# Kernel optimization log

Measured on AMD Instinct MI355X. Metric: run time of the kernel, lower is better.

## Reference

```python
import jax, jax.numpy as jnp
import numpy as np

N = 50000          # num nodes
E = 800000         # num edges (before self loops)
F = 128            # input feature dim
UNITS = 128        # output units
ATT_UNITS = 128    # attention units (Q/K dim)
HEADS = 8


def setup_inputs() -> dict:
    key = jax.random.key(0)
    ks = jax.random.split(key, 6)
    s = 1.0 / np.sqrt(F).astype(np.float32)  # ~glorot scale
    return {
        "x": jax.random.normal(ks[0], (N, F), dtype=jnp.float32),
        "edge_index": jax.random.randint(ks[1], (2, E), 0, N, dtype=jnp.int32),
        "query_kernel": jax.random.normal(ks[2], (F, ATT_UNITS), dtype=jnp.float32) * s,
        "query_bias": jnp.zeros((ATT_UNITS,), jnp.float32),
        "key_kernel": jax.random.normal(ks[3], (F, ATT_UNITS), dtype=jnp.float32) * s,
        "key_bias": jnp.zeros((ATT_UNITS,), jnp.float32),
        "kernel": jax.random.normal(ks[4], (F, UNITS), dtype=jnp.float32) * s,
        "bias": jnp.zeros((UNITS,), jnp.float32),
    }


def segment_softmax(scores, seg, num_segments):
    # scores: [E', H], seg: [E'] -> softmax over edges sharing the same target node, per head
    smax = jax.ops.segment_max(scores, seg, num_segments=num_segments)
    sexp = jnp.exp(scores - smax[seg])
    ssum = jax.ops.segment_sum(sexp, seg, num_segments=num_segments)
    return sexp / ssum[seg]


def reference(x, edge_index, query_kernel, query_bias, key_kernel, key_bias, kernel, bias):
    num_nodes = x.shape[0]
    # add self-loop edges (as in tf_geometric add_self_loop_edge)
    loop = jnp.arange(num_nodes, dtype=edge_index.dtype)
    row = jnp.concatenate([edge_index[0], loop])  # target nodes, [E']
    col = jnp.concatenate([edge_index[1], loop])  # source nodes, [E']

    Q = jax.nn.relu(x @ query_kernel + query_bias)[row]  # [E', A]
    K = jax.nn.relu(x @ key_kernel + key_bias)[col]      # [E', A]
    V = (x @ kernel)[col]                                 # [E', U]

    # split into attention heads: tf.split(..., num_heads, axis=-1)
    Qh = Q.reshape(-1, HEADS, ATT_UNITS // HEADS)
    Kh = K.reshape(-1, HEADS, ATT_UNITS // HEADS)
    att = jnp.sum(Qh * Kh, axis=-1)                       # [E', H]
    alpha = segment_softmax(att, row, num_nodes)          # [E', H]

    # split_value_heads=True: split V into head slices, weight, scatter-add, concat
    Vh = V.reshape(-1, HEADS, UNITS // HEADS)             # [E', H, U/H]
    msg = Vh * alpha[:, :, None]
    out = jax.ops.segment_sum(msg, row, num_segments=num_nodes)  # [N, H, U/H]
    out = out.reshape(num_nodes, UNITS)
    out = out + bias  # use_bias=True, activation=None
    return out
```

## Files before the change

kernel.cpp:

```cpp
#include <hip/hip_runtime.h>
#include <hip/hip_fp16.h>
#include <cstdint>

#define FDIM 128
#define XSTR 136
#define NROWTILE 128
#define WCHUNKS ((FDIM * XSTR * 2) / 1024)
#define CSRS 128

typedef __attribute__((ext_vector_type(8))) _Float16 half8;
typedef __attribute__((ext_vector_type(2))) _Float16 h2;
typedef __attribute__((ext_vector_type(16))) float float16;

#if defined(__has_builtin)
#if __has_builtin(__builtin_amdgcn_fdot2)
#define HAVE_FDOT2 1
#endif
#endif

__device__ __forceinline__ void gload_lds16(const void* g, void* s) {
    __builtin_amdgcn_global_load_lds(
        (const __attribute__((address_space(1))) void*)g,
        (__attribute__((address_space(3))) void*)s, 16, 0, 0);
}

__device__ __forceinline__ h2 as_h2(unsigned u) {
    union { unsigned u; h2 h; } c; c.u = u; return c.h;
}
__device__ __forceinline__ float2 h2_to_f2(unsigned u) {
    __half2 h = *(__half2*)&u;
    return __half22float2(h);
}

__global__ __launch_bounds__(256) void prep_k(
    const float* __restrict__ Wq, const float* __restrict__ Wk,
    const float* __restrict__ Wv, __half* __restrict__ WTH,
    int* __restrict__ deg, int N)
{
    int idx = blockIdx.x * 256 + threadIdx.x;

    if (idx < N) deg[idx] = 0;

    if (idx < 3 * FDIM * FDIM) {
        int mat = idx >> 14;
        int m = idx & 16383;
        int k = m >> 7;
        int nn = m & 127;
        const float* __restrict__ W = (mat == 0) ? Wq : (mat == 1) ? Wk : Wv;
        WTH[(size_t)mat * FDIM * XSTR + nn * XSTR + k] =
            __float2half_rn(W[k * FDIM + nn]);
    }
}

__global__ __launch_bounds__(256) void gemm_edges_k(
    const float* __restrict__ x, const __half* __restrict__ WTH,
    const float* __restrict__ bq, const float* __restrict__ bk,
    const float* __restrict__ bias,
    __half* __restrict__ Qb, uint2* __restrict__ KV,
    const int* __restrict__ ei, int E,
    int* __restrict__ deg, int* __restrict__ csr, int N)
{
    __shared__ __half xs[NROWTILE * XSTR];
    __shared__ __half ws[FDIM * XSTR];

    const int tid  = threadIdx.x;
    const int wave = tid >> 6;
    const int lane = tid & 63;
    const int r0   = blockIdx.x * NROWTILE;

    for (int c = wave; c < WCHUNKS; c += 4)
        gload_lds16((const char*)WTH + c * 1024 + lane * 16, (char*)ws + c * 1024);

    #pragma unroll
    for (int it = 0; it < 16; ++it) {
        int idx = it * 256 + tid;
        int row = idx >> 5;
        int c = (idx & 31) << 2;
        float4 v = make_float4(0.f, 0.f, 0.f, 0.f);
        if (r0 + row < N) v = *(const float4*)(x + (size_t)(r0 + row) * FDIM + c);
        __half h[4] = {__float2half_rn(v.x), __float2half_rn(v.y),
                       __float2half_rn(v.z), __float2half_rn(v.w)};
        *(ushort4*)(xs + row * XSTR + c) = *(ushort4*)h;
    }

    {
        const int NT = gridDim.x * 256;
        const int gtid = blockIdx.x * 256 + tid;
        for (int e = gtid; e < E; e += NT) {
            int row = ei[e];
            int col = ei[E + e];
            int slot = atomicAdd(&deg[row], 1);
            if (slot < CSRS) csr[(row << 7) + slot] = col;
        }
    }

    const int mrow = lane & 31;
    const int half = lane >> 5;
    const int arow = wave * 32 + mrow;

    for (int mat = 0; mat < 3; ++mat) {
        __syncthreads();

        float16 acc[4];
        #pragma unroll
        for (int nt = 0; nt < 4; ++nt)
            #pragma unroll
            for (int r = 0; r < 16; ++r) acc[nt][r] = 0.f;

        #pragma unroll
        for (int ks = 0; ks < 8; ++ks) {
            const int ko = ks * 16 + half * 8;
            half8 ah = *(const half8*)(xs + arow * XSTR + ko);
            #pragma unroll
            for (int nt = 0; nt < 4; ++nt) {
                half8 bh = *(const half8*)(ws + (nt * 32 + mrow) * XSTR + ko);
                acc[nt] = __builtin_amdgcn_mfma_f32_32x32x16_f16(ah, bh, acc[nt], 0, 0, 0);
            }
        }

        __syncthreads();

        const float* bvec = (mat == 0) ? bq : (mat == 1) ? bk : bias;
        #pragma unroll
        for (int nt = 0; nt < 4; ++nt) {
            const int col = nt * 32 + mrow;
            const float bb = bvec[col];
            #pragma unroll
            for (int reg = 0; reg < 16; ++reg) {
                int rl = wave * 32 + (reg & 3) + 8 * (reg >> 2) + 4 * half;
                float v = acc[nt][reg] + bb;
                if (mat < 2) v = fmaxf(v, 0.f);
                ws[rl * XSTR + col] = __float2half_rn(v);
            }
        }
        __syncthreads();

        if (mat == 0) {
            #pragma unroll
            for (int it = 0; it < 8; ++it) {
                int idx = it * 256 + tid;
                int row = idx >> 4;
                int c = (idx & 15) * 8;
                uint4 v = *(const uint4*)(ws + row * XSTR + c);
                if (r0 + row < N)
                    *(uint4*)(Qb + (size_t)(r0 + row) * FDIM + c) = v;
            }
        } else {
            __half* kvh = (__half*)KV;
            const int sub = (mat == 2) ? 2 : 0;
            #pragma unroll
            for (int it = 0; it < 32; ++it) {
                int idx = it * 256 + tid;
                int row = idx >> 6;
                int p = idx & 63;
                unsigned v = *(const unsigned*)(ws + row * XSTR + 2 * p);
                if (r0 + row < N)
                    *(unsigned*)(kvh + (size_t)(r0 + row) * 256 + p * 4 + sub) = v;
            }
        }
        __syncthreads();

        if (mat < 2) {
            const char* wbase = (const char*)(WTH + (size_t)(mat + 1) * FDIM * XSTR);
            for (int c = wave; c < WCHUNKS; c += 4)
                gload_lds16(wbase + c * 1024 + lane * 16, (char*)ws + c * 1024);
        }
    }
}

__global__ __launch_bounds__(256) void aggregate_k(
    const __half* __restrict__ Qb, const uint2* __restrict__ KV,
    const int* __restrict__ deg, const int* __restrict__ csr,
    float* __restrict__ out, int N)
{
    const int lane = threadIdx.x & 63;
    int n = blockIdx.x * 4 + (threadIdx.x >> 6);
    if (n >= N) return;
    n = __builtin_amdgcn_readfirstlane(n);

    int d = __builtin_amdgcn_readfirstlane(deg[n]);
    if (d > CSRS) d = CSRS;
    const int off   = n << 7;
    const int total = d + 1;

    const unsigned qu = *(const unsigned*)(Qb + (size_t)n * FDIM + 2 * lane);
    const h2 q2 = as_h2(qu);
#ifndef HAVE_FDOT2
    const float2 qf = h2_to_f2(qu);
#endif

    float acc0 = 0.f, acc1 = 0.f, lsum = 0.f;

    int idxbuf[8];
    #pragma unroll
    for (int u = 0; u < 8; ++u)
        idxbuf[u] = (u == 0) ? n : ((u < total) ? csr[off + u - 1] : 0);

    for (int t = 0; t < total; t += 8) {
        uint2 kv[8];
        #pragma unroll
        for (int u = 0; u < 8; ++u)
            kv[u] = KV[(((unsigned)idxbuf[u]) << 6) + lane];
        #pragma unroll
        for (int u = 0; u < 8; ++u) {
            int nx = t + 8 + u;
            idxbuf[u] = (nx < total) ? csr[off + nx - 1] : 0;
        }
        #pragma unroll
        for (int u = 0; u < 8; ++u) {
#ifdef HAVE_FDOT2
            float p = __builtin_amdgcn_fdot2(as_h2(kv[u].x), q2, 0.0f, false);
#else
            float2 kf = h2_to_f2(kv[u].x);
            float p = qf.x * kf.x + qf.y * kf.y;
#endif
            p += __shfl_xor(p, 1);
            p += __shfl_xor(p, 2);
            p += __shfl_xor(p, 4);
            float s = (t + u < total) ? __expf(p) : 0.f;
            float2 vf = h2_to_f2(kv[u].y);
            lsum += s;
            acc0 += s * vf.x;
            acc1 += s * vf.y;
        }
    }

    const float inv = 1.0f / lsum;
    float2 o;
    o.x = acc0 * inv;
    o.y = acc1 * inv;
    *(float2*)(out + (size_t)n * FDIM + 2 * lane) = o;
}

extern "C" void kernel_launch(void* const* d_in, const int* in_sizes, int n_in,
                              void* d_out, int out_size, void* d_ws, size_t ws_size,
                              hipStream_t stream)
{
    const float* x    = (const float*)d_in[0];
    const int*   ei   = (const int*)d_in[1];
    const float* Wq   = (const float*)d_in[2];
    const float* bq   = (const float*)d_in[3];
    const float* Wk   = (const float*)d_in[4];
    const float* bk   = (const float*)d_in[5];
    const float* Wv   = (const float*)d_in[6];
    const float* bias = (const float*)d_in[7];
    float* out = (float*)d_out;

    const int N = in_sizes[0] / FDIM;
    const int E = in_sizes[1] / 2;
    const int nblk = (N + NROWTILE - 1) / NROWTILE;

    __half* WTH = (__half*)d_ws;
    __half* Qb  = WTH + (size_t)3 * FDIM * XSTR;
    uint2*  KV  = (uint2*)(Qb + (size_t)N * FDIM);
    int* deg    = (int*)(KV + (size_t)N * 64);
    int* csr    = deg + N;

    int prep_n = N > 3 * FDIM * FDIM ? N : 3 * FDIM * FDIM;
    prep_k<<<(prep_n + 255) / 256, 256, 0, stream>>>(Wq, Wk, Wv, WTH, deg, N);

    gemm_edges_k<<<nblk, 256, 0, stream>>>(
        x, WTH, bq, bk, bias, Qb, KV, ei, E, deg, csr, N);

    aggregate_k<<<(N + 3) / 4, 256, 0, stream>>>(Qb, KV, deg, csr, out, N);
}
```

Measured before the change: 205.5 us.

## Move CSR edge scatter into dedicated extra blocks with batched atomics

Edge bucketing (atomic degree increment plus CSR write) moves out of the GEMM blocks into SBLK extra blocks appended to the same grid. Those blocks handle eight edges per thread per iteration, issuing the loads, then the atomics, then the stores in batches so more memory operations are in flight. The GEMM blocks no longer wait on the atomic scatter before their MFMA work, so the two tasks can run concurrently on different CUs. The risk is that the scatter blocks are scheduled after the GEMM blocks, or that a 120-block split leaves the scatter work unbalanced.

```diff
diff --git a/kernel.cpp b/kernel.cpp
--- a/kernel.cpp
+++ b/kernel.cpp
@@ -7,6 +7,7 @@
 #define NROWTILE 128
 #define WCHUNKS ((FDIM * XSTR * 2) / 1024)
 #define CSRS 128
+#define SBLK 120
 
 typedef __attribute__((ext_vector_type(8))) _Float16 half8;
 typedef __attribute__((ext_vector_type(2))) _Float16 h2;
@@ -58,12 +59,37 @@
     const float* __restrict__ bias,
     __half* __restrict__ Qb, uint2* __restrict__ KV,
     const int* __restrict__ ei, int E,
-    int* __restrict__ deg, int* __restrict__ csr, int N)
+    int* __restrict__ deg, int* __restrict__ csr, int N, int nblk)
 {
     __shared__ __half xs[NROWTILE * XSTR];
     __shared__ __half ws[FDIM * XSTR];
 
     const int tid  = threadIdx.x;
+
+    if ((int)blockIdx.x >= nblk) {
+        const int sb  = blockIdx.x - nblk;
+        const int t0  = sb * 256 + tid;
+        const int NTH = SBLK * 256;
+        for (int base = t0; base < E; base += NTH * 8) {
+            int er[8], ec[8], sl[8];
+            #pragma unroll
+            for (int u = 0; u < 8; ++u) {
+                int e = base + u * NTH;
+                bool v = (e < E);
+                er[u] = v ? ei[e] : -1;
+                ec[u] = v ? ei[E + e] : 0;
+            }
+            #pragma unroll
+            for (int u = 0; u < 8; ++u)
+                if (er[u] >= 0) sl[u] = atomicAdd(&deg[er[u]], 1);
+            #pragma unroll
+            for (int u = 0; u < 8; ++u)
+                if (er[u] >= 0 && sl[u] < CSRS)
+                    csr[(er[u] << 7) + sl[u]] = ec[u];
+        }
+        return;
+    }
+
     const int wave = tid >> 6;
     const int lane = tid & 63;
     const int r0   = blockIdx.x * NROWTILE;
@@ -83,17 +109,6 @@
         *(ushort4*)(xs + row * XSTR + c) = *(ushort4*)h;
     }
 
-    {
-        const int NT = gridDim.x * 256;
-        const int gtid = blockIdx.x * 256 + tid;
-        for (int e = gtid; e < E; e += NT) {
-            int row = ei[e];
-            int col = ei[E + e];
-            int slot = atomicAdd(&deg[row], 1);
-            if (slot < CSRS) csr[(row << 7) + slot] = col;
-        }
-    }
-
     const int mrow = lane & 31;
     const int half = lane >> 5;
     const int arow = wave * 32 + mrow;
@@ -259,8 +274,8 @@
     int prep_n = N > 3 * FDIM * FDIM ? N : 3 * FDIM * FDIM;
     prep_k<<<(prep_n + 255) / 256, 256, 0, stream>>>(Wq, Wk, Wv, WTH, deg, N);
 
-    gemm_edges_k<<<nblk, 256, 0, stream>>>(
-        x, WTH, bq, bk, bias, Qb, KV, ei, E, deg, csr, N);
+    gemm_edges_k<<<nblk + SBLK, 256, 0, stream>>>(
+        x, WTH, bq, bk, bias, Qb, KV, ei, E, deg, csr, N, nblk);
 
     aggregate_k<<<(N + 3) / 4, 256, 0, stream>>>(Qb, KV, deg, csr, out, N);
 }
```

Result: faster. 197.8 us (-3.8%).
